# Performance work log

Hardware: AMD Instinct MI355X
Metric: run time of the kernel (lower is better)

The kernel has to match this reference:

```python
import jax, jax.numpy as jnp
import numpy as np

N_COLS = 107
CAT_SLICES = [(1, 10), (10, 26), (27, 34), (34, 49), (49, 55), (55, 60), (60, 62), (65, 107)]
MSE_COLS = [0, 26, 62, 63, 64]
BATCH = 524288


def setup_inputs() -> dict:
    key = jax.random.key(0)
    k_dec, k_cont, k_cat = jax.random.split(key, 3)
    data_decoded = jax.random.normal(k_dec, (BATCH, N_COLS), dtype=jnp.float32)
    # Build data_true: continuous cols random, categorical slices exactly one-hot.
    data_true = jax.random.uniform(k_cont, (BATCH, N_COLS), dtype=jnp.float32)
    rows = jnp.arange(BATCH)
    for i, (s, e) in enumerate(CAT_SLICES):
        kk = jax.random.fold_in(k_cat, i)
        labels = jax.random.randint(kk, (BATCH,), 0, e - s)
        data_true = data_true.at[:, s:e].set(0.0)
        data_true = data_true.at[rows, s + labels].set(1.0)
    return {"data_decoded": data_decoded, "data_true": data_true, "batch_size": BATCH}


def _ce(logits, onehot_true):
    # torch nonzero()[:,1] on an exact one-hot slice == argmax
    labels = jnp.argmax(onehot_true, axis=1)
    logp = jax.nn.log_softmax(logits, axis=1)
    return -jnp.mean(jnp.take_along_axis(logp, labels[:, None], axis=1))


def _mse(a, b):
    d = a - b
    return jnp.mean(d * d)


def reference(data_decoded, data_true, batch_size):
    mse_loss = jnp.float32(0.0)
    for c in MSE_COLS:
        mse_loss = mse_loss + _mse(data_decoded[:, c], data_true[:, c])
    ce_loss = jnp.float32(0.0)
    for s, e in CAT_SLICES:
        ce_loss = ce_loss + _ce(data_decoded[:, s:e], data_true[:, s:e])
    multi_loss = mse_loss + ce_loss
    return multi_loss, mse_loss, ce_loss
```

## Files before the change

### kernel.cpp

```cpp
#include <hip/hip_runtime.h>

#define NCOLS 107
#define GROUP_F4 107
#define THREADS 256
#define BN 4
#define GROUPS_PER_BLOCK 128

typedef float f4 __attribute__((ext_vector_type(4)));

__device__ __host__ __forceinline__ constexpr int nbat(int cnt) {
    return (cnt + BN - 1) / BN;
}
__device__ __host__ __forceinline__ constexpr int blen(int b, int cnt) {
    return (BN * (b + 1) <= cnt) ? BN : (cnt - BN * b);
}

__device__ __host__ __forceinline__ constexpr int slice_of(int col) {
    return (col >= 1  && col < 10) ? 0 :
           (col >= 10 && col < 26) ? 1 :
           (col >= 27 && col < 34) ? 2 :
           (col >= 34 && col < 49) ? 3 :
           (col >= 49 && col < 55) ? 4 :
           (col >= 55 && col < 60) ? 5 :
           (col >= 60 && col < 62) ? 6 :
           (col >= 65)             ? 7 : -1;
}
__device__ __host__ __forceinline__ constexpr int slice_last(int sid) {
    return sid == 0 ?  9 : sid == 1 ? 25 : sid == 2 ? 33 : sid == 3 ? 48 :
           sid == 4 ? 54 : sid == 5 ? 59 : sid == 6 ? 61 : 106;
}

template<int L>
__device__ __forceinline__ void elem(float d, float t, float (&s)[8],
                                     float& mse, float& dot, float& lse,
                                     float& hs, float& ts) {
    constexpr int col = L % NCOLS;
    constexpr int sid = slice_of(col);
    if constexpr (L == 215) {
        hs += __expf(d);
        dot = __builtin_fmaf(d, t, dot);
    } else if constexpr (L >= 216 && L <= 223) {
        ts += __expf(d);
        dot = __builtin_fmaf(d, t, dot);
    } else if constexpr (sid < 0) {
        float df = d - t;
        mse += df * df;
    } else {
        s[sid] += __expf(d);
        dot = __builtin_fmaf(d, t, dot);
        if constexpr (col == slice_last(sid)) {
            lse += __logf(s[sid]);
            s[sid] = 0.0f;
        }
    }
}

template<int C0, int CNT, int B, int K = 0>
__device__ __forceinline__ void bload(const f4* __restrict__ gd,
                                      const f4* __restrict__ gt,
                                      f4 (&d)[BN], f4 (&t)[BN]) {
    if constexpr (K < blen(B, CNT)) {
        d[K] = gd[C0 + B * BN + K];
        t[K] = gt[C0 + B * BN + K];
        bload<C0, CNT, B, K + 1>(gd, gt, d, t);
    }
}

template<int C0, int CNT, int B, int K = 0>
__device__ __forceinline__ void bproc(const f4 (&d)[BN], const f4 (&t)[BN],
                                      float (&s)[8], float& mse, float& dot,
                                      float& lse, float& hs, float& ts) {
    if constexpr (K < blen(B, CNT)) {
        constexpr int C = C0 + B * BN + K;
        elem<4 * C + 0>(d[K][0], t[K][0], s, mse, dot, lse, hs, ts);
        elem<4 * C + 1>(d[K][1], t[K][1], s, mse, dot, lse, hs, ts);
        elem<4 * C + 2>(d[K][2], t[K][2], s, mse, dot, lse, hs, ts);
        elem<4 * C + 3>(d[K][3], t[K][3], s, mse, dot, lse, hs, ts);
        bproc<C0, CNT, B, K + 1>(d, t, s, mse, dot, lse, hs, ts);
    }
}

template<int C0, int CNT, int B>
__device__ __forceinline__ void stage(const f4* __restrict__ gd,
                                      const f4* __restrict__ gt,
                                      f4 (&d0)[BN], f4 (&t0)[BN],
                                      f4 (&d1)[BN], f4 (&t1)[BN],
                                      f4 (&d2)[BN], f4 (&t2)[BN],
                                      float (&s)[8], float& mse, float& dot,
                                      float& lse, float& hs, float& ts) {
    f4 d3[BN], t3[BN];
    if constexpr (B + 3 < nbat(CNT)) {
        bload<C0, CNT, B + 3>(gd, gt, d3, t3);
        __builtin_amdgcn_sched_barrier(0);
    }
    bproc<C0, CNT, B>(d0, t0, s, mse, dot, lse, hs, ts);
    if constexpr (B + 1 < nbat(CNT)) {
        stage<C0, CNT, B + 1>(gd, gt, d1, t1, d2, t2, d3, t3,
                              s, mse, dot, lse, hs, ts);
    }
}

template<int C0, int CNT>
__device__ __forceinline__ void run(const f4* __restrict__ gd,
                                    const f4* __restrict__ gt,
                                    float (&s)[8], float& mse, float& dot,
                                    float& lse, float& hs, float& ts) {
    f4 ad[BN], at[BN], bd[BN], bt[BN], cd[BN], ct[BN];
    bload<C0, CNT, 0>(gd, gt, ad, at);
    bload<C0, CNT, 1>(gd, gt, bd, bt);
    bload<C0, CNT, 2>(gd, gt, cd, ct);
    stage<C0, CNT, 0>(gd, gt, ad, at, bd, bt, cd, ct, s, mse, dot, lse, hs, ts);
}

__global__ __launch_bounds__(THREADS, 4) void multiloss_main(
        const float* __restrict__ dec, const float* __restrict__ tru,
        float2* __restrict__ ws) {
    __shared__ float headlds[GROUPS_PER_BLOCK];
    int lane = threadIdx.x & 63;
    int wid  = threadIdx.x >> 6;
    int half = wid >> 1;
    int gloc = (wid & 1) * 64 + lane;
    int g    = blockIdx.x * GROUPS_PER_BLOCK + gloc;

    float mse = 0.0f, dot = 0.0f, lse = 0.0f, hs = 0.0f, ts = 0.0f;
    float s[8] = {0.0f, 0.0f, 0.0f, 0.0f, 0.0f, 0.0f, 0.0f, 0.0f};
    const f4* gd = (const f4*)dec + (size_t)g * GROUP_F4;
    const f4* gt = (const f4*)tru + (size_t)g * GROUP_F4;

    if (half == 0) {
        run<0, 54>(gd, gt, s, mse, dot, lse, hs, ts);
        headlds[gloc] = hs;
    } else {
        run<54, 53>(gd, gt, s, mse, dot, lse, hs, ts);
    }
    __syncthreads();
    if (half == 1)
        lse += __logf(headlds[gloc] + ts);

    float ce = lse - dot;
#pragma unroll
    for (int off = 32; off > 0; off >>= 1) {
        mse += __shfl_down(mse, off, 64);
        ce  += __shfl_down(ce,  off, 64);
    }
    if (lane == 0)
        ws[blockIdx.x * 4 + wid] = make_float2(mse, ce);
}

__global__ __launch_bounds__(256) void multiloss_fin(
        const float2* __restrict__ ws, float* __restrict__ out,
        int nslots, float invN) {
    float m = 0.0f, c = 0.0f;
    for (int i = threadIdx.x; i < nslots; i += 256) {
        float2 v = ws[i];
        m += v.x; c += v.y;
    }
#pragma unroll
    for (int off = 32; off > 0; off >>= 1) {
        m += __shfl_down(m, off, 64);
        c += __shfl_down(c, off, 64);
    }
    __shared__ float sm[4], sc[4];
    int wid  = threadIdx.x >> 6;
    int lane = threadIdx.x & 63;
    if (lane == 0) { sm[wid] = m; sc[wid] = c; }
    __syncthreads();
    if (threadIdx.x == 0) {
        float mse = (sm[0] + sm[1] + sm[2] + sm[3]) * invN;
        float ce  = (sc[0] + sc[1] + sc[2] + sc[3]) * invN;
        out[0] = mse + ce;
        out[1] = mse;
        out[2] = ce;
    }
}

extern "C" void kernel_launch(void* const* d_in, const int* in_sizes, int n_in,
                              void* d_out, int out_size, void* d_ws, size_t ws_size,
                              hipStream_t stream) {
    const float* dec = (const float*)d_in[0];
    const float* tru = (const float*)d_in[1];
    int nrows   = in_sizes[0] / NCOLS;
    int ngroups = nrows / 4;
    int nblocks = ngroups / GROUPS_PER_BLOCK;
    int nwaves  = nblocks * 4;
    float2* ws = (float2*)d_ws;
    multiloss_main<<<nblocks, THREADS, 0, stream>>>(dec, tru, ws);
    multiloss_fin<<<1, 256, 0, stream>>>(ws, (float*)d_out, nwaves,
                                         1.0f / (float)nrows);
}
```

Baseline: 528.6 us.

## Realign half-split to slice boundary and drop LDS exchange; shrink prefetch depth

The per-thread column split between the two wave halves moves from 54/53 to 56/51 float4s. Because the split now lands on a categorical slice boundary, no softmax slice spans both halves. That removes the shared-memory partial-sum exchange, the __syncthreads and the special-case head/tail accumulators. The load pipeline also shrinks from three batches of four float4s to two batches of three, which cuts register pressure but leaves fewer loads in flight. The two halves now do unequal amounts of work, which may add a little imbalance.

```diff
diff --git a/kernel.cpp b/kernel.cpp
--- a/kernel.cpp
+++ b/kernel.cpp
@@ -3,7 +3,7 @@
 #define NCOLS 107
 #define GROUP_F4 107
 #define THREADS 256
-#define BN 4
+#define BN 3
 #define GROUPS_PER_BLOCK 128
 
 typedef float f4 __attribute__((ext_vector_type(4)));
@@ -32,17 +32,10 @@
 
 template<int L>
 __device__ __forceinline__ void elem(float d, float t, float (&s)[8],
-                                     float& mse, float& dot, float& lse,
-                                     float& hs, float& ts) {
+                                     float& mse, float& dot, float& lse) {
     constexpr int col = L % NCOLS;
     constexpr int sid = slice_of(col);
-    if constexpr (L == 215) {
-        hs += __expf(d);
-        dot = __builtin_fmaf(d, t, dot);
-    } else if constexpr (L >= 216 && L <= 223) {
-        ts += __expf(d);
-        dot = __builtin_fmaf(d, t, dot);
-    } else if constexpr (sid < 0) {
+    if constexpr (sid < 0) {
         float df = d - t;
         mse += df * df;
     } else {
@@ -68,15 +61,15 @@
 
 template<int C0, int CNT, int B, int K = 0>
 __device__ __forceinline__ void bproc(const f4 (&d)[BN], const f4 (&t)[BN],
-                                      float (&s)[8], float& mse, float& dot,
-                                      float& lse, float& hs, float& ts) {
+                                      float (&s)[8],
+                                      float& mse, float& dot, float& lse) {
     if constexpr (K < blen(B, CNT)) {
         constexpr int C = C0 + B * BN + K;
-        elem<4 * C + 0>(d[K][0], t[K][0], s, mse, dot, lse, hs, ts);
-        elem<4 * C + 1>(d[K][1], t[K][1], s, mse, dot, lse, hs, ts);
-        elem<4 * C + 2>(d[K][2], t[K][2], s, mse, dot, lse, hs, ts);
-        elem<4 * C + 3>(d[K][3], t[K][3], s, mse, dot, lse, hs, ts);
-        bproc<C0, CNT, B, K + 1>(d, t, s, mse, dot, lse, hs, ts);
+        elem<4 * C + 0>(d[K][0], t[K][0], s, mse, dot, lse);
+        elem<4 * C + 1>(d[K][1], t[K][1], s, mse, dot, lse);
+        elem<4 * C + 2>(d[K][2], t[K][2], s, mse, dot, lse);
+        elem<4 * C + 3>(d[K][3], t[K][3], s, mse, dot, lse);
+        bproc<C0, CNT, B, K + 1>(d, t, s, mse, dot, lse);
     }
 }
 
@@ -85,57 +78,49 @@
                                       const f4* __restrict__ gt,
                                       f4 (&d0)[BN], f4 (&t0)[BN],
                                       f4 (&d1)[BN], f4 (&t1)[BN],
-                                      f4 (&d2)[BN], f4 (&t2)[BN],
-                                      float (&s)[8], float& mse, float& dot,
-                                      float& lse, float& hs, float& ts) {
-    f4 d3[BN], t3[BN];
-    if constexpr (B + 3 < nbat(CNT)) {
-        bload<C0, CNT, B + 3>(gd, gt, d3, t3);
+                                      float (&s)[8],
+                                      float& mse, float& dot, float& lse) {
+    f4 d2[BN], t2[BN];
+    if constexpr (B + 2 < nbat(CNT)) {
+        bload<C0, CNT, B + 2>(gd, gt, d2, t2);
         __builtin_amdgcn_sched_barrier(0);
     }
-    bproc<C0, CNT, B>(d0, t0, s, mse, dot, lse, hs, ts);
+    bproc<C0, CNT, B>(d0, t0, s, mse, dot, lse);
     if constexpr (B + 1 < nbat(CNT)) {
-        stage<C0, CNT, B + 1>(gd, gt, d1, t1, d2, t2, d3, t3,
-                              s, mse, dot, lse, hs, ts);
+        stage<C0, CNT, B + 1>(gd, gt, d1, t1, d2, t2, s, mse, dot, lse);
     }
 }
 
 template<int C0, int CNT>
 __device__ __forceinline__ void run(const f4* __restrict__ gd,
                                     const f4* __restrict__ gt,
-                                    float (&s)[8], float& mse, float& dot,
-                                    float& lse, float& hs, float& ts) {
-    f4 ad[BN], at[BN], bd[BN], bt[BN], cd[BN], ct[BN];
+                                    float (&s)[8],
+                                    float& mse, float& dot, float& lse) {
+    f4 ad[BN], at[BN], bd[BN], bt[BN];
     bload<C0, CNT, 0>(gd, gt, ad, at);
     bload<C0, CNT, 1>(gd, gt, bd, bt);
-    bload<C0, CNT, 2>(gd, gt, cd, ct);
-    stage<C0, CNT, 0>(gd, gt, ad, at, bd, bt, cd, ct, s, mse, dot, lse, hs, ts);
+    stage<C0, CNT, 0>(gd, gt, ad, at, bd, bt, s, mse, dot, lse);
 }
 
 __global__ __launch_bounds__(THREADS, 4) void multiloss_main(
         const float* __restrict__ dec, const float* __restrict__ tru,
         float2* __restrict__ ws) {
-    __shared__ float headlds[GROUPS_PER_BLOCK];
     int lane = threadIdx.x & 63;
     int wid  = threadIdx.x >> 6;
     int half = wid >> 1;
     int gloc = (wid & 1) * 64 + lane;
     int g    = blockIdx.x * GROUPS_PER_BLOCK + gloc;
 
-    float mse = 0.0f, dot = 0.0f, lse = 0.0f, hs = 0.0f, ts = 0.0f;
+    float mse = 0.0f, dot = 0.0f, lse = 0.0f;
     float s[8] = {0.0f, 0.0f, 0.0f, 0.0f, 0.0f, 0.0f, 0.0f, 0.0f};
     const f4* gd = (const f4*)dec + (size_t)g * GROUP_F4;
     const f4* gt = (const f4*)tru + (size_t)g * GROUP_F4;
 
     if (half == 0) {
-        run<0, 54>(gd, gt, s, mse, dot, lse, hs, ts);
-        headlds[gloc] = hs;
+        run<0, 56>(gd, gt, s, mse, dot, lse);
     } else {
-        run<54, 53>(gd, gt, s, mse, dot, lse, hs, ts);
+        run<56, 51>(gd, gt, s, mse, dot, lse);
     }
-    __syncthreads();
-    if (half == 1)
-        lse += __logf(headlds[gloc] + ts);
 
     float ce = lse - dot;
 #pragma unroll
```

New measurement: 478.0 us. -9.6%, faster.
